# Optimization experiments

Measured on AMD Instinct MI355X. Metric: run time of the kernel, lower is better.

## Reference

```python
import jax, jax.numpy as jnp
import numpy as np

K_DELTA = 2.0
K_AN = 2.0
N_CLASSES = 32


def _masked_mean(x, mask):
    m = mask.astype(x.dtype)
    return jnp.sum(x * m) / jnp.maximum(jnp.sum(m), 1.0)


def setup_inputs() -> dict:
    key = jax.random.key(0)
    k1, k2 = jax.random.split(key)
    logits = jax.random.normal(k1, (384, 1024), dtype=jnp.float32)
    labels = jax.random.randint(k2, (384,), 0, N_CLASSES)
    return {"logits": logits, "labels": labels}


def reference(logits, labels):
    # Faithful jit-safe translation: torch.where / torch.unique produce
    # dynamic-shaped index lists; here we return the equivalent boolean
    # masks over the full triplet / pair space instead.
    N = labels.shape[0]
    x = jax.lax.stop_gradient(logits)  # logits.detach()
    x = x / jnp.linalg.norm(x, axis=1, keepdims=True)  # F.normalize p=2 dim=1
    mat = -(x @ x.T)  # negative cosine similarity, symmetric [N, N]

    sames = labels[:, None] == labels[None, :]
    diffs = ~sames
    sames = sames & ~jnp.eye(N, dtype=bool)  # fill_diagonal_(0)
    # triplet validity mask over (anchor, positive, negative)
    trip = sames[:, :, None] & diffs[:, None, :]  # [N, N, N]

    # delta[a, p, n] = an_dist - ap_dist
    delta = mat[:, None, :] - mat[:, :, None]  # [N, N, N]

    # --- calc_loss_an branch: unique (anchor, negative) pairs ---
    # a pair (a, n) appears in some triplet iff diffs[a, n] and anchor a has
    # at least one positive; unique_filter canonicalizes to (min, max).
    has_pos = jnp.any(sames, axis=1)  # [N]
    upper = jnp.triu(jnp.ones((N, N), dtype=bool), k=1)
    pair_mask = upper & diffs & (has_pos[:, None] | has_pos[None, :])
    an_mean = _masked_mean(mat, pair_mask)
    beta = 1.0 + (-an_mean - 1.0) / K_AN  # self.update(an_dist_unique, 'an')
    an_pairs = pair_mask & (-mat >= beta)

    # --- epsilon update + semi-hard triplet selection ---
    eps = jnp.clip(_masked_mean(delta, trip) / K_DELTA, 0.0, 0.5)
    cond = trip & (delta <= eps) & (delta > 0.0)  # semi-hard

    return cond, an_pairs, eps, beta
```

## Files before the change

### kernel.cpp

```cpp
#include <hip/hip_runtime.h>
#include <stdint.h>

#define N 384
#define D 1024
#define N2 (N * N)
static constexpr size_t N3 = (size_t)N * N2;

static constexpr size_t PART_OFF = 0;
static constexpr size_t MAT_OFF  = 4718592;
static constexpr size_t INVN_OFF = 5898240;
static constexpr size_t TN_OFF   = 5901312;
static constexpr size_t TC_OFF   = 5904384;
static constexpr size_t ANS_OFF  = 5907456;
static constexpr size_t ANC_OFF  = 5910528;
static constexpr size_t HP_OFF   = 5913600;

static constexpr int GEMM_BLOCKS = 576;
static constexpr int NORM_BLOCKS = 96;
static constexpr int FILL_BLOCKS = 2048;
static constexpr int FILL_F4     = 14192640;

__global__ __launch_bounds__(256) void k_mega(const float* __restrict__ x,
                                              double* __restrict__ part,
                                              double* __restrict__ invn,
                                              float4* __restrict__ outv) {
  __shared__ double As[64][32];
  __shared__ double Bs[64][32];
  int b = blockIdx.x;
  int t = threadIdx.x;

  if (b >= GEMM_BLOCKS + NORM_BLOCKS) {
    int i = (b - GEMM_BLOCKS - NORM_BLOCKS) * 256 + t;
    const int stride = FILL_BLOCKS * 256;
    const float4 z = make_float4(0.f, 0.f, 0.f, 0.f);
    for (; i < FILL_F4; i += stride) outv[i] = z;
    return;
  }
  if (b >= GEMM_BLOCKS) {
    int w = t >> 6, lane = t & 63;
    int a = (b - GEMM_BLOCKS) * 4 + w;
    const float4* row = (const float4*)(x + (size_t)a * D);
    double s = 0.0;
#pragma unroll
    for (int j = 0; j < 4; ++j) {
      float4 v = row[lane + 64 * j];
      double dx = v.x, dy = v.y, dz = v.z, dw = v.w;
      s += dx * dx + dy * dy + dz * dz + dw * dw;
    }
#pragma unroll
    for (int m = 32; m; m >>= 1) s += __shfl_xor(s, m, 64);
    if (lane == 0) invn[a] = 1.0 / sqrt(s);
    return;
  }

  int bz = b / 144, rem = b % 144;
  int m0 = (rem % 12) * 32, n0 = (rem / 12) * 32, k0 = bz * 256;
  int tm = t & 15, tn = t >> 4;
  double a00 = 0, a01 = 0, a10 = 0, a11 = 0;
  for (int kc = 0; kc < 4; ++kc) {
    int kbase = k0 + kc * 64;
#pragma unroll
    for (int h = 0; h < 2; ++h) {
      int f = t + h * 256;
      int m = f & 31, kq = f >> 5;
      float4 va = *(const float4*)(x + (size_t)(m0 + m) * D + kbase + kq * 4);
      As[kq * 4 + 0][m] = (double)va.x; As[kq * 4 + 1][m] = (double)va.y;
      As[kq * 4 + 2][m] = (double)va.z; As[kq * 4 + 3][m] = (double)va.w;
      float4 vb = *(const float4*)(x + (size_t)(n0 + m) * D + kbase + kq * 4);
      Bs[kq * 4 + 0][m] = (double)vb.x; Bs[kq * 4 + 1][m] = (double)vb.y;
      Bs[kq * 4 + 2][m] = (double)vb.z; Bs[kq * 4 + 3][m] = (double)vb.w;
    }
    __syncthreads();
#pragma unroll 8
    for (int k = 0; k < 64; ++k) {
      double ax = As[k][2 * tm], ay = As[k][2 * tm + 1];
      double bx = Bs[k][2 * tn], by = Bs[k][2 * tn + 1];
      a00 = fma(ax, bx, a00);
      a01 = fma(ax, by, a01);
      a10 = fma(ay, bx, a10);
      a11 = fma(ay, by, a11);
    }
    __syncthreads();
  }
  double* o = part + (size_t)bz * N2;
  int r0 = m0 + 2 * tm, c0 = n0 + 2 * tn;
  o[(size_t)r0 * N + c0]           = a00;
  o[(size_t)r0 * N + c0 + 1]       = a01;
  o[(size_t)(r0 + 1) * N + c0]     = a10;
  o[(size_t)(r0 + 1) * N + c0 + 1] = a11;
}

__global__ __launch_bounds__(384) void k_stats(const double* __restrict__ part,
                                               const double* __restrict__ invn,
                                               const int* __restrict__ labels,
                                               double* __restrict__ mat,
                                               double* __restrict__ tn,
                                               double* __restrict__ tc,
                                               double* __restrict__ ans,
                                               double* __restrict__ anc,
                                               int* __restrict__ hp) {
  __shared__ int labs[N];
  __shared__ int hist[32];
  __shared__ double cw[6][6];
  int a = blockIdx.x, t = threadIdx.x;
  int w = t >> 6, lane = t & 63;
  if (t < 32) hist[t] = 0;
  labs[t] = labels[t];
  __syncthreads();
  atomicAdd(&hist[labs[t] & 31], 1);
  __syncthreads();
  int la = labs[a];
  size_t idx = (size_t)a * N + t;
  double s = part[idx];
  s += part[(size_t)N2 + idx];
  s += part[2 * (size_t)N2 + idx];
  s += part[3 * (size_t)N2 + idx];
  double m = -(s * (invn[a] * invn[t]));
  mat[idx] = m;
  bool same = (labs[t] == la) && (t != a);
  bool diff = (labs[t] != la);
  bool hpa = hist[la] >= 2;
  bool hpt = hist[labs[t]] >= 2;
  bool anm = (t > a) && diff && (hpa || hpt);

  double q[6];
  q[0] = same ? m : 0.0;
  q[1] = same ? 1.0 : 0.0;
  q[2] = diff ? m : 0.0;
  q[3] = diff ? 1.0 : 0.0;
  q[4] = anm ? m : 0.0;
  q[5] = anm ? 1.0 : 0.0;
#pragma unroll
  for (int i = 0; i < 6; ++i) {
#pragma unroll
    for (int s2 = 32; s2; s2 >>= 1) q[i] += __shfl_xor(q[i], s2, 64);
  }
  if (lane == 0) {
#pragma unroll
    for (int i = 0; i < 6; ++i) cw[w][i] = q[i];
  }
  __syncthreads();
  if (t == 0) {
    double r[6];
#pragma unroll
    for (int i = 0; i < 6; ++i) {
      double s3 = 0.0;
      for (int ww = 0; ww < 6; ++ww) s3 += cw[ww][i];
      r[i] = s3;
    }
    tn[a]  = r[2] * r[1] - r[0] * r[3];
    tc[a]  = r[1] * r[3];
    ans[a] = r[4];
    anc[a] = r[5];
    hp[a]  = hpa ? 1 : 0;
  }
}

__global__ __launch_bounds__(256) void k_sparse(const double* __restrict__ mat,
                                                const int* __restrict__ labels,
                                                const int* __restrict__ hp,
                                                const double* __restrict__ tn,
                                                const double* __restrict__ tc,
                                                const double* __restrict__ ans,
                                                const double* __restrict__ anc,
                                                float* __restrict__ out) {
  __shared__ int labs[N];
  __shared__ int hpL[N];
  __shared__ double matA[N];
  __shared__ int list[N];
  __shared__ int cnt;
  __shared__ double sEps, sBeta;
  int a = blockIdx.x, t = threadIdx.x;
  for (int i = t; i < N; i += 256) {
    labs[i] = labels[i];
    hpL[i] = hp[i];
    matA[i] = mat[(size_t)a * N + i];
  }
  if (t == 0) cnt = 0;
  if (t < 64) {
    double vtn = 0, vtc = 0, vas = 0, vac = 0;
#pragma unroll
    for (int j = 0; j < 6; ++j) {
      int idx = t + 64 * j;
      vtn += tn[idx]; vtc += tc[idx]; vas += ans[idx]; vac += anc[idx];
    }
#pragma unroll
    for (int s = 32; s; s >>= 1) {
      vtn += __shfl_xor(vtn, s, 64);
      vtc += __shfl_xor(vtc, s, 64);
      vas += __shfl_xor(vas, s, 64);
      vac += __shfl_xor(vac, s, 64);
    }
    if (t == 0) {
      double an_mean = vas / fmax(vac, 1.0);
      double beta = 1.0 + ((-an_mean) - 1.0) / 2.0;
      double em = vtn / fmax(vtc, 1.0);
      double eps = em / 2.0;
      eps = eps < 0.0 ? 0.0 : (eps > 0.5 ? 0.5 : eps);
      sEps = eps;
      sBeta = beta;
      if (a == 0) {
        out[N3 + N2]     = (float)eps;
        out[N3 + N2 + 1] = (float)beta;
      }
    }
  }
  __syncthreads();
  int la = labs[a];
  for (int i = t; i < N; i += 256) {
    if (labs[i] == la && i != a) list[atomicAdd(&cnt, 1)] = i;
  }
  __syncthreads();
  double eps = sEps, beta = sBeta;
  int hpa = hpL[a];
  if (t < 96) {
    int b0 = t * 4;
    float r[4];
#pragma unroll
    for (int j = 0; j < 4; ++j) {
      int b = b0 + j;
      bool pm = (a < b) && (labs[b] != la) && (hpa || hpL[b]);
      r[j] = (pm && (-matA[b] >= beta)) ? 1.0f : 0.0f;
    }
    *((float4*)(out + N3 + (size_t)a * N + b0)) =
        make_float4(r[0], r[1], r[2], r[3]);
  }
  int nc = cnt;
  for (int base = 0; base < nc; base += 2) {
    int rr = base + (t / 96);
    if (t < 192 && rr < nc) {
      int p = list[rr];
      double mp = matA[p];
      int n0 = (t % 96) * 4;
      float r[4];
#pragma unroll
      for (int j = 0; j < 4; ++j) {
        int n = n0 + j;
        double d = matA[n] - mp;
        r[j] = ((labs[n] != la) && (d > 0.0) && (d <= eps)) ? 1.0f : 0.0f;
      }
      *((float4*)(out + (size_t)a * N2 + (size_t)p * N + n0)) =
          make_float4(r[0], r[1], r[2], r[3]);
    }
  }
}

extern "C" void kernel_launch(void* const* d_in, const int* in_sizes, int n_in,
                              void* d_out, int out_size, void* d_ws, size_t ws_size,
                              hipStream_t stream) {
  const float* logits = (const float*)d_in[0];
  const int* labels = (const int*)d_in[1];
  float* out = (float*)d_out;
  char* ws = (char*)d_ws;
  double* part = (double*)(ws + PART_OFF);
  double* mat  = (double*)(ws + MAT_OFF);
  double* invn = (double*)(ws + INVN_OFF);
  double* tn   = (double*)(ws + TN_OFF);
  double* tc   = (double*)(ws + TC_OFF);
  double* ans  = (double*)(ws + ANS_OFF);
  double* anc  = (double*)(ws + ANC_OFF);
  int* hp      = (int*)(ws + HP_OFF);

  k_mega<<<dim3(GEMM_BLOCKS + NORM_BLOCKS + FILL_BLOCKS), dim3(256), 0,
           stream>>>(logits, part, invn, (float4*)out);
  k_stats<<<dim3(N), dim3(384), 0, stream>>>(part, invn, labels, mat, tn, tc,
                                             ans, anc, hp);
  k_sparse<<<dim3(N), dim3(256), 0, stream>>>(mat, labels, hp, tn, tc, ans,
                                              anc, out);
}
```

Before: 52.47 us.

## Fuse stats and sparse kernels into one tail kernel with grid barrier

Merges the stats and sparse-write kernels into a single 192-block kernel. Each block handles two anchor rows, keeps the normalized similarity rows in shared memory instead of writing and rereading a global mat buffer, and waits on an atomic-counter grid barrier before the global eps/beta reduction. This removes one kernel launch and the mat round trip through global memory. The spin barrier depends on all 192 blocks being resident at once, and the counter is reset inside the previous kernel.

```diff
diff --git a/kernel.cpp b/kernel.cpp
--- a/kernel.cpp
+++ b/kernel.cpp
@@ -7,22 +7,26 @@
 static constexpr size_t N3 = (size_t)N * N2;
 
 static constexpr size_t PART_OFF = 0;
-static constexpr size_t MAT_OFF  = 4718592;
-static constexpr size_t INVN_OFF = 5898240;
-static constexpr size_t TN_OFF   = 5901312;
-static constexpr size_t TC_OFF   = 5904384;
-static constexpr size_t ANS_OFF  = 5907456;
-static constexpr size_t ANC_OFF  = 5910528;
-static constexpr size_t HP_OFF   = 5913600;
+static constexpr size_t INVN_OFF = 4718592;
+static constexpr size_t TN_OFF   = 4721664;
+static constexpr size_t TC_OFF   = 4724736;
+static constexpr size_t ANS_OFF  = 4727808;
+static constexpr size_t ANC_OFF  = 4730880;
+static constexpr size_t HP_OFF   = 4733952;
+static constexpr size_t SYNC_OFF = 4735488;
 
 static constexpr int GEMM_BLOCKS = 576;
 static constexpr int NORM_BLOCKS = 96;
 static constexpr int FILL_BLOCKS = 2048;
 static constexpr int FILL_F4     = 14192640;
+static constexpr int TAIL_BLOCKS = 192;
+
+#define AGT __HIP_MEMORY_SCOPE_AGENT
 
 __global__ __launch_bounds__(256) void k_mega(const float* __restrict__ x,
                                               double* __restrict__ part,
                                               double* __restrict__ invn,
+                                              int* __restrict__ sync,
                                               float4* __restrict__ outv) {
   __shared__ double As[64][32];
   __shared__ double Bs[64][32];
@@ -37,6 +41,8 @@
     return;
   }
   if (b >= GEMM_BLOCKS) {
+    if (b == GEMM_BLOCKS && t == 0)
+      __hip_atomic_store(sync, 0, __ATOMIC_RELAXED, AGT);
     int w = t >> 6, lane = t & 63;
     int a = (b - GEMM_BLOCKS) * 4 + w;
     const float4* row = (const float4*)(x + (size_t)a * D);
@@ -90,99 +96,100 @@
   o[(size_t)(r0 + 1) * N + c0 + 1] = a11;
 }
 
-__global__ __launch_bounds__(384) void k_stats(const double* __restrict__ part,
-                                               const double* __restrict__ invn,
-                                               const int* __restrict__ labels,
-                                               double* __restrict__ mat,
-                                               double* __restrict__ tn,
-                                               double* __restrict__ tc,
-                                               double* __restrict__ ans,
-                                               double* __restrict__ anc,
-                                               int* __restrict__ hp) {
+__global__ __launch_bounds__(384) void k_tail(const double* __restrict__ part,
+                                              const double* __restrict__ invn,
+                                              const int* __restrict__ labels,
+                                              double* __restrict__ tn,
+                                              double* __restrict__ tc,
+                                              double* __restrict__ ans,
+                                              double* __restrict__ anc,
+                                              int* __restrict__ hp,
+                                              int* __restrict__ sync,
+                                              float* __restrict__ out) {
   __shared__ int labs[N];
   __shared__ int hist[32];
   __shared__ double cw[6][6];
-  int a = blockIdx.x, t = threadIdx.x;
+  __shared__ double matX[2][N];
+  __shared__ int hpL[N];
+  __shared__ int list[N];
+  __shared__ int cnt;
+  __shared__ double sEps, sBeta;
+  int t = threadIdx.x;
   int w = t >> 6, lane = t & 63;
   if (t < 32) hist[t] = 0;
   labs[t] = labels[t];
   __syncthreads();
   atomicAdd(&hist[labs[t] & 31], 1);
   __syncthreads();
-  int la = labs[a];
-  size_t idx = (size_t)a * N + t;
-  double s = part[idx];
-  s += part[(size_t)N2 + idx];
-  s += part[2 * (size_t)N2 + idx];
-  s += part[3 * (size_t)N2 + idx];
-  double m = -(s * (invn[a] * invn[t]));
-  mat[idx] = m;
-  bool same = (labs[t] == la) && (t != a);
-  bool diff = (labs[t] != la);
-  bool hpa = hist[la] >= 2;
-  bool hpt = hist[labs[t]] >= 2;
-  bool anm = (t > a) && diff && (hpa || hpt);
-
-  double q[6];
-  q[0] = same ? m : 0.0;
-  q[1] = same ? 1.0 : 0.0;
-  q[2] = diff ? m : 0.0;
-  q[3] = diff ? 1.0 : 0.0;
-  q[4] = anm ? m : 0.0;
-  q[5] = anm ? 1.0 : 0.0;
-#pragma unroll
-  for (int i = 0; i < 6; ++i) {
-#pragma unroll
-    for (int s2 = 32; s2; s2 >>= 1) q[i] += __shfl_xor(q[i], s2, 64);
-  }
-  if (lane == 0) {
-#pragma unroll
-    for (int i = 0; i < 6; ++i) cw[w][i] = q[i];
-  }
-  __syncthreads();
+
+  for (int half = 0; half < 2; ++half) {
+    int a = blockIdx.x + half * TAIL_BLOCKS;
+    int la = labs[a];
+    size_t idx = (size_t)a * N + t;
+    double s = part[idx];
+    s += part[(size_t)N2 + idx];
+    s += part[2 * (size_t)N2 + idx];
+    s += part[3 * (size_t)N2 + idx];
+    double m = -(s * (invn[a] * invn[t]));
+    matX[half][t] = m;
+    bool same = (labs[t] == la) && (t != a);
+    bool diff = (labs[t] != la);
+    bool hpa = hist[la] >= 2;
+    bool hpt = hist[labs[t]] >= 2;
+    bool anm = (t > a) && diff && (hpa || hpt);
+
+    double q[6];
+    q[0] = same ? m : 0.0;
+    q[1] = same ? 1.0 : 0.0;
+    q[2] = diff ? m : 0.0;
+    q[3] = diff ? 1.0 : 0.0;
+    q[4] = anm ? m : 0.0;
+    q[5] = anm ? 1.0 : 0.0;
+#pragma unroll
+    for (int i = 0; i < 6; ++i) {
+#pragma unroll
+      for (int s2 = 32; s2; s2 >>= 1) q[i] += __shfl_xor(q[i], s2, 64);
+    }
+    if (lane == 0) {
+#pragma unroll
+      for (int i = 0; i < 6; ++i) cw[w][i] = q[i];
+    }
+    __syncthreads();
+    if (t == 0) {
+      double r[6];
+#pragma unroll
+      for (int i = 0; i < 6; ++i) {
+        double s3 = 0.0;
+        for (int ww = 0; ww < 6; ++ww) s3 += cw[ww][i];
+        r[i] = s3;
+      }
+      __hip_atomic_store(&tn[a],  r[2] * r[1] - r[0] * r[3], __ATOMIC_RELAXED, AGT);
+      __hip_atomic_store(&tc[a],  r[1] * r[3], __ATOMIC_RELAXED, AGT);
+      __hip_atomic_store(&ans[a], r[4], __ATOMIC_RELAXED, AGT);
+      __hip_atomic_store(&anc[a], r[5], __ATOMIC_RELAXED, AGT);
+      __hip_atomic_store(&hp[a],  hpa ? 1 : 0, __ATOMIC_RELAXED, AGT);
+    }
+    __syncthreads();
+  }
+
   if (t == 0) {
-    double r[6];
-#pragma unroll
-    for (int i = 0; i < 6; ++i) {
-      double s3 = 0.0;
-      for (int ww = 0; ww < 6; ++ww) s3 += cw[ww][i];
-      r[i] = s3;
-    }
-    tn[a]  = r[2] * r[1] - r[0] * r[3];
-    tc[a]  = r[1] * r[3];
-    ans[a] = r[4];
-    anc[a] = r[5];
-    hp[a]  = hpa ? 1 : 0;
-  }
-}
-
-__global__ __launch_bounds__(256) void k_sparse(const double* __restrict__ mat,
-                                                const int* __restrict__ labels,
-                                                const int* __restrict__ hp,
-                                                const double* __restrict__ tn,
-                                                const double* __restrict__ tc,
-                                                const double* __restrict__ ans,
-                                                const double* __restrict__ anc,
-                                                float* __restrict__ out) {
-  __shared__ int labs[N];
-  __shared__ int hpL[N];
-  __shared__ double matA[N];
-  __shared__ int list[N];
-  __shared__ int cnt;
-  __shared__ double sEps, sBeta;
-  int a = blockIdx.x, t = threadIdx.x;
-  for (int i = t; i < N; i += 256) {
-    labs[i] = labels[i];
-    hpL[i] = hp[i];
-    matA[i] = mat[(size_t)a * N + i];
-  }
-  if (t == 0) cnt = 0;
+    __threadfence();
+    atomicAdd(sync, 1);
+    while (__hip_atomic_load(sync, __ATOMIC_RELAXED, AGT) < TAIL_BLOCKS) {}
+    __threadfence();
+  }
+  __syncthreads();
+
+  hpL[t] = __hip_atomic_load(&hp[t], __ATOMIC_RELAXED, AGT);
   if (t < 64) {
     double vtn = 0, vtc = 0, vas = 0, vac = 0;
 #pragma unroll
     for (int j = 0; j < 6; ++j) {
       int idx = t + 64 * j;
-      vtn += tn[idx]; vtc += tc[idx]; vas += ans[idx]; vac += anc[idx];
+      vtn += __hip_atomic_load(&tn[idx],  __ATOMIC_RELAXED, AGT);
+      vtc += __hip_atomic_load(&tc[idx],  __ATOMIC_RELAXED, AGT);
+      vas += __hip_atomic_load(&ans[idx], __ATOMIC_RELAXED, AGT);
+      vac += __hip_atomic_load(&anc[idx], __ATOMIC_RELAXED, AGT);
     }
 #pragma unroll
     for (int s = 32; s; s >>= 1) {
@@ -199,49 +206,54 @@
       eps = eps < 0.0 ? 0.0 : (eps > 0.5 ? 0.5 : eps);
       sEps = eps;
       sBeta = beta;
-      if (a == 0) {
+      if (blockIdx.x == 0) {
         out[N3 + N2]     = (float)eps;
         out[N3 + N2 + 1] = (float)beta;
       }
     }
   }
   __syncthreads();
-  int la = labs[a];
-  for (int i = t; i < N; i += 256) {
-    if (labs[i] == la && i != a) list[atomicAdd(&cnt, 1)] = i;
-  }
-  __syncthreads();
   double eps = sEps, beta = sBeta;
-  int hpa = hpL[a];
-  if (t < 96) {
-    int b0 = t * 4;
-    float r[4];
-#pragma unroll
-    for (int j = 0; j < 4; ++j) {
-      int b = b0 + j;
-      bool pm = (a < b) && (labs[b] != la) && (hpa || hpL[b]);
-      r[j] = (pm && (-matA[b] >= beta)) ? 1.0f : 0.0f;
-    }
-    *((float4*)(out + N3 + (size_t)a * N + b0)) =
-        make_float4(r[0], r[1], r[2], r[3]);
-  }
-  int nc = cnt;
-  for (int base = 0; base < nc; base += 2) {
-    int rr = base + (t / 96);
-    if (t < 192 && rr < nc) {
-      int p = list[rr];
-      double mp = matA[p];
-      int n0 = (t % 96) * 4;
+
+  for (int half = 0; half < 2; ++half) {
+    int a = blockIdx.x + half * TAIL_BLOCKS;
+    int la = labs[a];
+    int hpa = hpL[a];
+    if (t == 0) cnt = 0;
+    __syncthreads();
+    if (labs[t] == la && t != a) list[atomicAdd(&cnt, 1)] = t;
+    __syncthreads();
+    if (t < 96) {
+      int b0 = t * 4;
       float r[4];
 #pragma unroll
       for (int j = 0; j < 4; ++j) {
-        int n = n0 + j;
-        double d = matA[n] - mp;
-        r[j] = ((labs[n] != la) && (d > 0.0) && (d <= eps)) ? 1.0f : 0.0f;
-      }
-      *((float4*)(out + (size_t)a * N2 + (size_t)p * N + n0)) =
+        int b = b0 + j;
+        bool pm = (a < b) && (labs[b] != la) && (hpa || hpL[b]);
+        r[j] = (pm && (-matX[half][b] >= beta)) ? 1.0f : 0.0f;
+      }
+      *((float4*)(out + N3 + (size_t)a * N + b0)) =
           make_float4(r[0], r[1], r[2], r[3]);
     }
+    int nc = cnt;
+    for (int base = 0; base < nc; base += 4) {
+      int rr = base + (t / 96);
+      if (rr < nc) {
+        int p = list[rr];
+        double mp = matX[half][p];
+        int n0 = (t % 96) * 4;
+        float r[4];
+#pragma unroll
+        for (int j = 0; j < 4; ++j) {
+          int n = n0 + j;
+          double d = matX[half][n] - mp;
+          r[j] = ((labs[n] != la) && (d > 0.0) && (d <= eps)) ? 1.0f : 0.0f;
+        }
+        *((float4*)(out + (size_t)a * N2 + (size_t)p * N + n0)) =
+            make_float4(r[0], r[1], r[2], r[3]);
+      }
+    }
+    __syncthreads();
   }
 }
 
@@ -253,18 +265,16 @@
   float* out = (float*)d_out;
   char* ws = (char*)d_ws;
   double* part = (double*)(ws + PART_OFF);
-  double* mat  = (double*)(ws + MAT_OFF);
   double* invn = (double*)(ws + INVN_OFF);
   double* tn   = (double*)(ws + TN_OFF);
   double* tc   = (double*)(ws + TC_OFF);
   double* ans  = (double*)(ws + ANS_OFF);
   double* anc  = (double*)(ws + ANC_OFF);
   int* hp      = (int*)(ws + HP_OFF);
+  int* sync    = (int*)(ws + SYNC_OFF);
 
   k_mega<<<dim3(GEMM_BLOCKS + NORM_BLOCKS + FILL_BLOCKS), dim3(256), 0,
-           stream>>>(logits, part, invn, (float4*)out);
-  k_stats<<<dim3(N), dim3(384), 0, stream>>>(part, invn, labels, mat, tn, tc,
-                                             ans, anc, hp);
-  k_sparse<<<dim3(N), dim3(256), 0, stream>>>(mat, labels, hp, tn, tc, ans,
-                                              anc, out);
+           stream>>>(logits, part, invn, sync, (float4*)out);
+  k_tail<<<dim3(TAIL_BLOCKS), dim3(384), 0, stream>>>(
+      part, invn, labels, tn, tc, ans, anc, hp, sync, out);
 }
```

Result: slower. 57.80 us (+10.2%).

## Fuse stats kernel into GEMM megakernel using a global atomic counter barrier

Applied to the files above, without the earlier changes.

Moves the row-norm computation into a small init kernel that also resets a sync counter, then folds the per-anchor stats stage into the megakernel. Stats blocks spin on a global counter until all GEMM blocks have published their partial products, which lets the stats work overlap with the zero-fill blocks. Each GEMM block issues a threadfence and an atomic increment when done. This trades one kernel launch boundary for spin-waiting blocks, and it depends on every GEMM block being scheduled before or alongside the waiting stats blocks, otherwise it could deadlock.

```diff
diff --git a/kernel.cpp b/kernel.cpp
--- a/kernel.cpp
+++ b/kernel.cpp
@@ -14,48 +14,136 @@
 static constexpr size_t ANS_OFF  = 5907456;
 static constexpr size_t ANC_OFF  = 5910528;
 static constexpr size_t HP_OFF   = 5913600;
+static constexpr size_t SYNC_OFF = 5915136;
 
 static constexpr int GEMM_BLOCKS = 576;
-static constexpr int NORM_BLOCKS = 96;
+static constexpr int STAT_BLOCKS = 384;
 static constexpr int FILL_BLOCKS = 2048;
 static constexpr int FILL_F4     = 14192640;
 
+#define AGT __HIP_MEMORY_SCOPE_AGENT
+
+__global__ __launch_bounds__(256) void k_init(const float* __restrict__ x,
+                                              double* __restrict__ invn,
+                                              int* __restrict__ sync) {
+  int b = blockIdx.x, t = threadIdx.x;
+  if (b == 96) {
+    if (t == 0) __hip_atomic_store(sync, 0, __ATOMIC_RELAXED, AGT);
+    return;
+  }
+  int w = t >> 6, lane = t & 63;
+  int a = b * 4 + w;
+  const float4* row = (const float4*)(x + (size_t)a * D);
+  double s = 0.0;
+#pragma unroll
+  for (int j = 0; j < 4; ++j) {
+    float4 v = row[lane + 64 * j];
+    double dx = v.x, dy = v.y, dz = v.z, dw = v.w;
+    s += dx * dx + dy * dy + dz * dz + dw * dw;
+  }
+#pragma unroll
+  for (int m = 32; m; m >>= 1) s += __shfl_xor(s, m, 64);
+  if (lane == 0) invn[a] = 1.0 / sqrt(s);
+}
+
 __global__ __launch_bounds__(256) void k_mega(const float* __restrict__ x,
+                                              const double* __restrict__ invn,
+                                              const int* __restrict__ labels,
                                               double* __restrict__ part,
-                                              double* __restrict__ invn,
+                                              double* __restrict__ mat,
+                                              double* __restrict__ tn,
+                                              double* __restrict__ tc,
+                                              double* __restrict__ ans,
+                                              double* __restrict__ anc,
+                                              int* __restrict__ hp,
+                                              int* __restrict__ sync,
                                               float4* __restrict__ outv) {
   __shared__ double As[64][32];
   __shared__ double Bs[64][32];
   int b = blockIdx.x;
   int t = threadIdx.x;
 
-  if (b >= GEMM_BLOCKS + NORM_BLOCKS) {
-    int i = (b - GEMM_BLOCKS - NORM_BLOCKS) * 256 + t;
+  if (b >= GEMM_BLOCKS + STAT_BLOCKS) {
+    int i = (b - GEMM_BLOCKS - STAT_BLOCKS) * 256 + t;
     const int stride = FILL_BLOCKS * 256;
     const float4 z = make_float4(0.f, 0.f, 0.f, 0.f);
     for (; i < FILL_F4; i += stride) outv[i] = z;
     return;
   }
+
   if (b >= GEMM_BLOCKS) {
+    __shared__ int labs[N];
+    __shared__ int hist[32];
+    __shared__ double cw[4][6];
+    int a = b - GEMM_BLOCKS;
+    for (int i = t; i < N; i += 256) labs[i] = labels[i];
+    if (t < 32) hist[t] = 0;
+    __syncthreads();
+    for (int i = t; i < N; i += 256) atomicAdd(&hist[labs[i] & 31], 1);
+    if (t == 0) {
+      while (__hip_atomic_load(sync, __ATOMIC_RELAXED, AGT) < GEMM_BLOCKS)
+        __builtin_amdgcn_s_sleep(8);
+      __threadfence();
+    }
+    __syncthreads();
+    int la = labs[a];
+    bool hpa = hist[la] >= 2;
+    double ia = invn[a];
+    double q[6] = {0, 0, 0, 0, 0, 0};
+#pragma unroll
+    for (int rep = 0; rep < 2; ++rep) {
+      int c = t + rep * 256;
+      if (c < N) {
+        size_t idx = (size_t)a * N + c;
+        double s = part[idx];
+        s += part[(size_t)N2 + idx];
+        s += part[2 * (size_t)N2 + idx];
+        s += part[3 * (size_t)N2 + idx];
+        double m = -(s * (ia * invn[c]));
+        mat[idx] = m;
+        bool same = (labs[c] == la) && (c != a);
+        bool diff = (labs[c] != la);
+        bool hpt = hist[labs[c]] >= 2;
+        bool anm = (c > a) && diff && (hpa || hpt);
+        q[0] += same ? m : 0.0;
+        q[1] += same ? 1.0 : 0.0;
+        q[2] += diff ? m : 0.0;
+        q[3] += diff ? 1.0 : 0.0;
+        q[4] += anm ? m : 0.0;
+        q[5] += anm ? 1.0 : 0.0;
+      }
+    }
     int w = t >> 6, lane = t & 63;
-    int a = (b - GEMM_BLOCKS) * 4 + w;
-    const float4* row = (const float4*)(x + (size_t)a * D);
-    double s = 0.0;
-#pragma unroll
-    for (int j = 0; j < 4; ++j) {
-      float4 v = row[lane + 64 * j];
-      double dx = v.x, dy = v.y, dz = v.z, dw = v.w;
-      s += dx * dx + dy * dy + dz * dz + dw * dw;
-    }
-#pragma unroll
-    for (int m = 32; m; m >>= 1) s += __shfl_xor(s, m, 64);
-    if (lane == 0) invn[a] = 1.0 / sqrt(s);
+#pragma unroll
+    for (int i = 0; i < 6; ++i) {
+#pragma unroll
+      for (int s2 = 32; s2; s2 >>= 1) q[i] += __shfl_xor(q[i], s2, 64);
+    }
+    if (lane == 0) {
+#pragma unroll
+      for (int i = 0; i < 6; ++i) cw[w][i] = q[i];
+    }
+    __syncthreads();
+    if (t == 0) {
+      double r[6];
+#pragma unroll
+      for (int i = 0; i < 6; ++i) {
+        double s3 = 0.0;
+        for (int ww = 0; ww < 4; ++ww) s3 += cw[ww][i];
+        r[i] = s3;
+      }
+      tn[a]  = r[2] * r[1] - r[0] * r[3];
+      tc[a]  = r[1] * r[3];
+      ans[a] = r[4];
+      anc[a] = r[5];
+      hp[a]  = hpa ? 1 : 0;
+    }
     return;
   }
 
   int bz = b / 144, rem = b % 144;
   int m0 = (rem % 12) * 32, n0 = (rem / 12) * 32, k0 = bz * 256;
-  int tm = t & 15, tn = t >> 4;
+  int tm = t & 15, tn_ = t >> 4;
   double a00 = 0, a01 = 0, a10 = 0, a11 = 0;
   for (int kc = 0; kc < 4; ++kc) {
     int kbase = k0 + kc * 64;
@@ -74,7 +162,7 @@
 #pragma unroll 8
     for (int k = 0; k < 64; ++k) {
       double ax = As[k][2 * tm], ay = As[k][2 * tm + 1];
-      double bx = Bs[k][2 * tn], by = Bs[k][2 * tn + 1];
+      double bx = Bs[k][2 * tn_], by = Bs[k][2 * tn_ + 1];
       a00 = fma(ax, bx, a00);
       a01 = fma(ax, by, a01);
       a10 = fma(ay, bx, a10);
@@ -83,77 +171,14 @@
     __syncthreads();
   }
   double* o = part + (size_t)bz * N2;
-  int r0 = m0 + 2 * tm, c0 = n0 + 2 * tn;
+  int r0 = m0 + 2 * tm, c0 = n0 + 2 * tn_;
   o[(size_t)r0 * N + c0]           = a00;
   o[(size_t)r0 * N + c0 + 1]       = a01;
   o[(size_t)(r0 + 1) * N + c0]     = a10;
   o[(size_t)(r0 + 1) * N + c0 + 1] = a11;
-}
-
-__global__ __launch_bounds__(384) void k_stats(const double* __restrict__ part,
-                                               const double* __restrict__ invn,
-                                               const int* __restrict__ labels,
-                                               double* __restrict__ mat,
-                                               double* __restrict__ tn,
-                                               double* __restrict__ tc,
-                                               double* __restrict__ ans,
-                                               double* __restrict__ anc,
-                                               int* __restrict__ hp) {
-  __shared__ int labs[N];
-  __shared__ int hist[32];
-  __shared__ double cw[6][6];
-  int a = blockIdx.x, t = threadIdx.x;
-  int w = t >> 6, lane = t & 63;
-  if (t < 32) hist[t] = 0;
-  labs[t] = labels[t];
+  __threadfence();
   __syncthreads();
-  atomicAdd(&hist[labs[t] & 31], 1);
-  __syncthreads();
-  int la = labs[a];
-  size_t idx = (size_t)a * N + t;
-  double s = part[idx];
-  s += part[(size_t)N2 + idx];
-  s += part[2 * (size_t)N2 + idx];
-  s += part[3 * (size_t)N2 + idx];
-  double m = -(s * (invn[a] * invn[t]));
-  mat[idx] = m;
-  bool same = (labs[t] == la) && (t != a);
-  bool diff = (labs[t] != la);
-  bool hpa = hist[la] >= 2;
-  bool hpt = hist[labs[t]] >= 2;
-  bool anm = (t > a) && diff && (hpa || hpt);
-
-  double q[6];
-  q[0] = same ? m : 0.0;
-  q[1] = same ? 1.0 : 0.0;
-  q[2] = diff ? m : 0.0;
-  q[3] = diff ? 1.0 : 0.0;
-  q[4] = anm ? m : 0.0;
-  q[5] = anm ? 1.0 : 0.0;
-#pragma unroll
-  for (int i = 0; i < 6; ++i) {
-#pragma unroll
-    for (int s2 = 32; s2; s2 >>= 1) q[i] += __shfl_xor(q[i], s2, 64);
-  }
-  if (lane == 0) {
-#pragma unroll
-    for (int i = 0; i < 6; ++i) cw[w][i] = q[i];
-  }
-  __syncthreads();
-  if (t == 0) {
-    double r[6];
-#pragma unroll
-    for (int i = 0; i < 6; ++i) {
-      double s3 = 0.0;
-      for (int ww = 0; ww < 6; ++ww) s3 += cw[ww][i];
-      r[i] = s3;
-    }
-    tn[a]  = r[2] * r[1] - r[0] * r[3];
-    tc[a]  = r[1] * r[3];
-    ans[a] = r[4];
-    anc[a] = r[5];
-    hp[a]  = hpa ? 1 : 0;
-  }
+  if (t == 0) atomicAdd(sync, 1);
 }
 
 __global__ __launch_bounds__(256) void k_sparse(const double* __restrict__ mat,
@@ -260,11 +285,12 @@
   double* ans  = (double*)(ws + ANS_OFF);
   double* anc  = (double*)(ws + ANC_OFF);
   int* hp      = (int*)(ws + HP_OFF);
-
-  k_mega<<<dim3(GEMM_BLOCKS + NORM_BLOCKS + FILL_BLOCKS), dim3(256), 0,
-           stream>>>(logits, part, invn, (float4*)out);
-  k_stats<<<dim3(N), dim3(384), 0, stream>>>(part, invn, labels, mat, tn, tc,
-                                             ans, anc, hp);
-  k_sparse<<<dim3(N), dim3(256), 0, stream>>>(mat, labels, hp, tn, tc, ans,
-                                              anc, out);
-}
+  int* sync    = (int*)(ws + SYNC_OFF);
+
+  k_init<<<dim3(97), dim3(256), 0, stream>>>(logits, invn, sync);
+  k_mega<<<dim3(GEMM_BLOCKS + STAT_BLOCKS + FILL_BLOCKS), dim3(256), 0,
+           stream>>>(logits, invn, labels, part, mat, tn, tc, ans, anc, hp,
+                     sync, (float4*)out);
+  k_sparse<<<dim3(STAT_BLOCKS), dim3(256), 0, stream>>>(
+      mat, labels, hp, tn, tc, ans, anc, out);
+}
```

Result: slower. 163.4 us (+211.5%).
